# Kernel optimization log

Measured on AMD Instinct MI355X. Metric: run time of the kernel, lower is better.

The kernel has to match this reference:

```python
import jax, jax.numpy as jnp
import numpy as np

B, S, D, H, KV, HD = 2, 2048, 4096, 32, 8, 128
N_REP = H // KV


def _rope(t, fr, fi):
    # t: [b, s, h, hd]; fr/fi: [s, hd//2] broadcast as [1, s, 1, hd//2]
    t2 = t.reshape(*t.shape[:-1], -1, 2)
    tr, ti = t2[..., 0], t2[..., 1]
    fr = fr[None, :, None, :]
    fi = fi[None, :, None, :]
    orr = tr * fr - fi * ti
    oi = tr * fi + ti * fr
    return jnp.stack([orr, oi], axis=-1).reshape(t.shape)


def setup_inputs() -> dict:
    key = jax.random.key(0)
    ks = jax.random.split(key, 8)
    scale = 0.02
    x = jax.random.normal(ks[0], (B, S, D), jnp.float32)
    wq = jax.random.normal(ks[1], (H * HD, D), jnp.float32) * scale
    wk = jax.random.normal(ks[2], (KV * HD, D), jnp.float32) * scale
    wv = jax.random.normal(ks[3], (KV * HD, D), jnp.float32) * scale
    wo = jax.random.normal(ks[4], (D, H * HD), jnp.float32) * scale
    # rotary frequencies (real/imag parts of freqs_cis)
    t = jnp.arange(S, dtype=jnp.float32)
    inv = 1.0 / (10000.0 ** (jnp.arange(0, HD, 2, dtype=jnp.float32) / HD))
    ang = t[:, None] * inv[None, :]  # [S, HD//2]
    fr, fi = jnp.cos(ang), jnp.sin(ang)
    # causal mask, additive
    mask = jnp.triu(jnp.full((S, S), -1e9, jnp.float32), 1)[None, None]
    cache_k = jnp.zeros((B, S, KV, HD), jnp.float32)
    cache_v = jnp.zeros((B, S, KV, HD), jnp.float32)
    indexes = jnp.arange(S, dtype=jnp.int32)
    cache_indexes = jnp.arange(S, dtype=jnp.int32)
    return dict(x=x, wq=wq, wk=wk, wv=wv, wo=wo, fr=fr, fi=fi, mask=mask,
                cache_k=cache_k, cache_v=cache_v, indexes=indexes,
                cache_indexes=cache_indexes)


def reference(x, wq, wk, wv, wo, fr, fi, mask, cache_k, cache_v, indexes, cache_indexes):
    bsz, seqlen, _ = x.shape
    xq = jnp.einsum('bsd,ed->bse', x, wq).reshape(bsz, seqlen, H, HD)
    xk = jnp.einsum('bsd,ed->bse', x, wk).reshape(bsz, seqlen, KV, HD)
    xv = jnp.einsum('bsd,ed->bse', x, wv).reshape(bsz, seqlen, KV, HD)
    xq = _rope(xq, fr, fi)
    xk = _rope(xk, fr, fi)
    # KV-cache scatter then gather
    cache_k = cache_k.at[:, indexes].set(xk)
    cache_v = cache_v.at[:, indexes].set(xv)
    keys = cache_k[:, cache_indexes]    # [b, kv_len, KV, hd]
    values = cache_v[:, cache_indexes]
    # GQA: repeat_interleave kv heads
    keys = jnp.repeat(keys, N_REP, axis=2)      # [b, kv_len, H, hd]
    values = jnp.repeat(values, N_REP, axis=2)
    q = xq.transpose(0, 2, 1, 3)        # [b, H, s, hd]
    k = keys.transpose(0, 2, 1, 3)      # [b, H, kv, hd]
    v = values.transpose(0, 2, 1, 3)
    scores = jnp.einsum('bhqd,bhkd->bhqk', q, k) / jnp.sqrt(jnp.float32(HD))
    scores = scores + mask
    probs = jax.nn.softmax(scores.astype(jnp.float32), axis=-1).astype(q.dtype)
    out = jnp.einsum('bhqk,bhkd->bhqd', probs, v)
    out = out.transpose(0, 2, 1, 3).reshape(bsz, seqlen, H * HD)
    out = jnp.einsum('bse,de->bsd', out, wo)
    return (out, xk, xv)
```

## Files before the change

kernel.cpp:

```cpp
#include <hip/hip_runtime.h>
#include <hip/hip_bf16.h>


typedef __attribute__((ext_vector_type(8)))  short s8v;
typedef __attribute__((ext_vector_type(4)))  short s4v;
typedef __attribute__((ext_vector_type(4)))  float f4v;
typedef __attribute__((ext_vector_type(16))) float f16v;
typedef __attribute__((ext_vector_type(2)))  float f2v;
typedef __attribute__((ext_vector_type(2))) unsigned int u2v;
typedef __attribute__((ext_vector_type(4))) unsigned int u4v;

typedef __attribute__((address_space(3))) void lds_void;
typedef __attribute__((address_space(1))) void g_void;

#define GLDS16(gp, lp) __builtin_amdgcn_global_load_lds((g_void*)(gp), (lds_void*)(lp), 16, 0, 0)

__device__ __forceinline__ unsigned short f2b(float f) {
  unsigned u = __builtin_bit_cast(unsigned, f);
  u += 0x7fffu + ((u >> 16) & 1u);
  return (unsigned short)(u >> 16);
}
__device__ __forceinline__ unsigned pk2(float a, float b) {
  return (unsigned)f2b(a) | ((unsigned)f2b(b) << 16);
}
__device__ __forceinline__ float b2f(unsigned short h) {
  return __builtin_bit_cast(float, (unsigned)h << 16);
}

__device__ __forceinline__ void mfma32(f4v& d, s8v a, s8v b) {
  asm volatile("v_mfma_f32_16x16x32_bf16 %0, %1, %2, %0" : "+v"(d) : "v"(a), "v"(b));
}
__device__ __forceinline__ void mfma3216(f16v& d, s8v a, s8v b) {
  asm volatile("v_mfma_f32_32x32x16_bf16 %0, %1, %2, %0" : "+v"(d) : "v"(a), "v"(b));
}
__device__ __forceinline__ s4v tr_read(const char* p, int imm) {
  s4v r;
  asm volatile("ds_read_b64_tr_b16 %0, %1 offset:%2"
               : "=v"(r) : "v"((lds_void*)p), "n"(imm));
  return r;
}

__global__ __launch_bounds__(256) void cvt_bf16(const float* __restrict__ s,
                                                unsigned short* __restrict__ d, int n4) {
  const int i = blockIdx.x * 256 + threadIdx.x;
  if (i >= n4) return;
  f4v v = *(const f4v*)(s + (size_t)i * 4);
  u2v r;
  r.x = pk2(v[0], v[1]);
  r.y = pk2(v[2], v[3]);
  *(u2v*)(d + (size_t)i * 4) = r;
}

#define BAR      asm volatile("s_barrier" ::: "memory")
#define WLGKM    do { asm volatile("s_waitcnt lgkmcnt(0)" ::: "memory"); \
                      __builtin_amdgcn_sched_barrier(0); } while (0)
#define WVM8     do { asm volatile("s_waitcnt vmcnt(8)" ::: "memory"); \
                      __builtin_amdgcn_sched_barrier(0); } while (0)

template <int OUTB>
__global__ __launch_bounds__(512, 2) void gemm_bt8(const unsigned short* __restrict__ A,
                                                   const unsigned short* __restrict__ Bp,
                                                   void* __restrict__ Cout,
                                                   int M, int N, int Ks, int Klen,
                                                   int nTiles) {
  __shared__ __align__(16) char smem[131072];
  const int tid = threadIdx.x, lane = tid & 63, wv = tid >> 6;
  const int qi = lane & 15, g = lane >> 4;
  const int wm = wv >> 2, wn = wv & 3;

  const int nwg = gridDim.x, cpx = nwg >> 3;
  const int id = blockIdx.x;
  const int swz = (id & 7) * cpx + (id >> 3);
  const int half = swz / nTiles;
  const int tile = swz - half * nTiles;
  const int kOff = half * Klen;
  const int MT = M >> 8;
  const int m0 = (tile % MT) * 256, n0 = (tile / MT) * 256;
  const int NT = Klen >> 6;

  const int srowo = wv * 8 + (lane >> 3);
  const int scole = ((lane & 7) ^ (lane >> 3)) << 3;
  const size_t rA = (size_t)(m0 + srowo) * Ks + kOff + scole;
  const size_t rB = (size_t)(n0 + srowo) * Ks + kOff + scole;
  char* sdA = smem + wv * 1024;
  char* sdB = smem + 32768 + wv * 1024;

#define STG_A(D, H, KT) do { \
    GLDS16(A + rA + (size_t)((H)*128) * Ks + (size_t)(KT)*64,      sdA + (D)*65536 + (H)*16384); \
    GLDS16(A + rA + (size_t)((H)*128 + 64) * Ks + (size_t)(KT)*64, sdA + (D)*65536 + (H)*16384 + 8192); } while (0)
#define STG_B(D, H, KT) do { \
    GLDS16(Bp + rB + (size_t)((H)*128) * Ks + (size_t)(KT)*64,      sdB + (D)*65536 + (H)*16384); \
    GLDS16(Bp + rB + (size_t)((H)*128 + 64) * Ks + (size_t)(KT)*64, sdB + (D)*65536 + (H)*16384 + 8192); } while (0)

  const int sw = (qi & 7) << 4;
  const char* frA = smem + (wm * 128 + qi) * 128;
  const char* frB = smem + 32768 + (wn * 64 + qi) * 128;

#define RDA4(D, F0) do { _Pragma("unroll") for (int f_ = 0; f_ < 4; ++f_) \
    _Pragma("unroll") for (int k_ = 0; k_ < 2; ++k_) \
      a[(F0) + f_][k_] = *(const s8v*)(frA + (D)*65536 + ((F0) + f_) * 2048 + (((k_ << 6) + (g << 4)) ^ sw)); } while (0)
#define RDB2(D, N0) do { _Pragma("unroll") for (int n_ = 0; n_ < 2; ++n_) \
    _Pragma("unroll") for (int k_ = 0; k_ < 2; ++k_) \
      b[(N0) + n_][k_] = *(const s8v*)(frB + (D)*65536 + ((N0) + n_) * 2048 + (((k_ << 6) + (g << 4)) ^ sw)); } while (0)
#define MQUAD(F0, N0) do { __builtin_amdgcn_s_setprio(1); \
    _Pragma("unroll") for (int f_ = 0; f_ < 4; ++f_) \
    _Pragma("unroll") for (int n_ = 0; n_ < 2; ++n_) \
    _Pragma("unroll") for (int k_ = 0; k_ < 2; ++k_) \
      mfma32(acc[(F0) + f_][(N0) + n_], a[(F0) + f_][k_], b[(N0) + n_][k_]); \
    __builtin_amdgcn_s_setprio(0); } while (0)

  f4v acc[8][4];
#pragma unroll
  for (int i = 0; i < 8; ++i)
#pragma unroll
    for (int j = 0; j < 4; ++j) acc[i][j] = (f4v)0.0f;

  STG_A(0, 0, 0); STG_A(0, 1, 0); STG_B(0, 0, 0); STG_B(0, 1, 0);
  STG_A(1, 0, 1); STG_A(1, 1, 1); STG_B(1, 0, 1); STG_B(1, 1, 1);
  WVM8;
  BAR;

  s8v a[8][2], b[4][2];
#pragma unroll 1
  for (int it = 0; it < NT / 2; ++it) {
    const int t = 2 * it;
    const int k2 = (t + 2 < NT) ? t + 2 : NT - 1;
    const int k3 = (t + 3 < NT) ? t + 3 : NT - 1;
    RDA4(0, 0); RDB2(0, 0);
    WLGKM; MQUAD(0, 0); BAR;
    RDB2(0, 2);
    WLGKM; MQUAD(0, 2); BAR;
    RDA4(0, 4);
    STG_B(0, 0, k2); STG_B(0, 1, k2);
    WLGKM; MQUAD(4, 0); BAR;
    STG_A(0, 0, k2); STG_A(0, 1, k2);
    MQUAD(4, 2);
    WVM8; BAR;
    RDA4(1, 0); RDB2(1, 0);
    WLGKM; MQUAD(0, 0); BAR;
    RDB2(1, 2);
    WLGKM; MQUAD(0, 2); BAR;
    RDA4(1, 4);
    STG_B(1, 0, k3); STG_B(1, 1, k3);
    WLGKM; MQUAD(4, 0); BAR;
    STG_A(1, 0, k3); STG_A(1, 1, k3);
    MQUAD(4, 2);
    WVM8; BAR;
  }

  asm volatile("s_waitcnt vmcnt(0)" ::: "memory");
  asm volatile("s_nop 7\n\ts_nop 7" ::: "memory");
  const int r4 = g * 4;
  if (OUTB) {
    unsigned short* Cb = (unsigned short*)Cout + (size_t)half * M * N;
#pragma unroll
    for (int fm = 0; fm < 8; ++fm)
#pragma unroll
      for (int fn = 0; fn < 4; ++fn)
#pragma unroll
        for (int r = 0; r < 4; ++r)
          Cb[(size_t)(m0 + wm * 128 + fm * 16 + r4 + r) * N + (n0 + wn * 64 + fn * 16 + qi)] =
              f2b(acc[fm][fn][r]);
  } else {
    float* Cf = (float*)Cout;
#pragma unroll
    for (int fm = 0; fm < 8; ++fm)
#pragma unroll
      for (int fn = 0; fn < 4; ++fn)
#pragma unroll
        for (int r = 0; r < 4; ++r)
          Cf[(size_t)(m0 + wm * 128 + fm * 16 + r4 + r) * N + (n0 + wn * 64 + fn * 16 + qi)] =
              acc[fm][fn][r];
  }
}

__global__ __launch_bounds__(256) void rope_scatter(
    const unsigned short* __restrict__ qkvp, const float* __restrict__ fr,
    const float* __restrict__ fi,
    unsigned short* __restrict__ qb, unsigned short* __restrict__ kb,
    unsigned short* __restrict__ vbuf, float* __restrict__ xk, float* __restrict__ xv) {
  const int idx = blockIdx.x * 256 + threadIdx.x;
  const int token = idx / 3072;
  const int col2  = (idx - token * 3072) * 2;
  const int pos   = token & 2047;
  const unsigned u1 = *(const unsigned*)(qkvp + (size_t)token * 6144 + col2);
  const unsigned u2 = *(const unsigned*)(qkvp + 25165824u + (size_t)token * 6144 + col2);
  float v0 = b2f((unsigned short)u1) + b2f((unsigned short)u2);
  float v1 = b2f((unsigned short)(u1 >> 16)) + b2f((unsigned short)(u2 >> 16));
  if (col2 < 4096) {
    const int j = (col2 & 127) >> 1;
    const float cr = fr[pos * 64 + j], ci = fi[pos * 64 + j];
    const float a = v0 * cr - ci * v1;
    const float o = v0 * ci + v1 * cr;
    *(unsigned*)(qb + (size_t)token * 4096 + col2) = pk2(a, o);
  } else if (col2 < 5120) {
    const int lc = col2 - 4096;
    const int j = (lc & 127) >> 1;
    const float cr = fr[pos * 64 + j], ci = fi[pos * 64 + j];
    const float a = v0 * cr - ci * v1;
    const float o = v0 * ci + v1 * cr;
    *(unsigned*)(kb + (size_t)token * 1024 + lc) = pk2(a, o);
    f2v w; w.x = a; w.y = o;
    *(f2v*)(xk + (size_t)token * 1024 + lc) = w;
  } else {
    const int lc = col2 - 5120;
    *(unsigned*)(vbuf + (size_t)token * 1024 + lc) = pk2(v0, v1);
    f2v w; w.x = v0; w.y = v1;
    *(f2v*)(xv + (size_t)token * 1024 + lc) = w;
  }
}

#define SCL_LOG2 0.12751744f

__global__ __launch_bounds__(512, 2) void attn_fwd(
    const unsigned short* __restrict__ qb, const unsigned short* __restrict__ kb,
    const unsigned short* __restrict__ vb, unsigned short* __restrict__ ao) {
  __shared__ __align__(16) char smem[49152];
  char* const Ks = smem;
  const int tid = threadIdx.x, lane = tid & 63, wv = tid >> 6;
  const int q31 = lane & 31, hi = lane >> 5;
  const int qtb = 7 - blockIdx.x;
  const int h = blockIdx.y, b = blockIdx.z, kvh = h >> 2;
  const int q0 = qtb * 256;
  const int qrow = q0 + wv * 32 + q31;

  s8v qf[8];
  {
    const unsigned short* qp = qb + (size_t)(b * 2048 + qrow) * 4096 + h * 128 + hi * 8;
#pragma unroll
    for (int c = 0; c < 8; ++c) qf[c] = *(const s8v*)(qp + c * 16);
  }

  f16v oacc[4];
#pragma unroll
  for (int i = 0; i < 4; ++i) oacc[i] = (f16v)0.0f;
  float m_run = -3.0e38f, l_run = 0.0f;

  const unsigned short* ksrc[2]; char* kdst[2];
#pragma unroll
  for (int j = 0; j < 2; ++j) {
    const int r = wv * 8 + j * 4 + (lane >> 4);
    ksrc[j] = kb + (size_t)(b * 2048 + r) * 1024 + kvh * 128 + (((lane & 15) ^ (r & 15)) << 3);
    kdst[j] = Ks + (wv * 8 + j * 4) * 256;
  }
  const unsigned short* vsrc[2]; int vdoff[2];
#pragma unroll
  for (int j = 0; j < 2; ++j) {
    const int key = (wv * 2 + j) * 4 + ((lane & 7) >> 1);
    const int d = ((lane >> 3) & 7) * 16 + (lane & 1) * 8;
    vsrc[j] = vb + (size_t)(b * 2048 + key) * 1024 + kvh * 128 + d;
    vdoff[j] = (wv * 16 + j * 8) * 128;
  }

  const int ntiles = 4 * qtb + 4;
  const int my_qmax = q0 + wv * 32 + 31, wq_lo = q0 + wv * 32;

  GLDS16(ksrc[0], kdst[0]); GLDS16(ksrc[1], kdst[1]);
  GLDS16(vsrc[0], smem + 16384 + vdoff[0]); GLDS16(vsrc[1], smem + 16384 + vdoff[1]);
  asm volatile("s_waitcnt vmcnt(2)" ::: "memory");
  __builtin_amdgcn_sched_barrier(0);
  BAR;

  for (int t = 0; t < ntiles; ++t) {
    const int k0 = t * 64;
    const bool live = (k0 <= my_qmax);
    f16v s32a = (f16v)0.0f, s32b = (f16v)0.0f;
    if (live) {
      __builtin_amdgcn_s_setprio(1);
#pragma unroll
      for (int c = 0; c < 8; ++c) {
        const int sl = ((2 * c + hi) ^ (q31 & 15)) << 4;
        s8v kfa = *(const s8v*)(Ks + q31 * 256 + sl);
        s8v kfb = *(const s8v*)(Ks + (32 + q31) * 256 + sl);
        mfma3216(s32a, kfa, qf[c]);
        mfma3216(s32b, kfb, qf[c]);
      }
      __builtin_amdgcn_s_setprio(0);
      asm volatile("s_nop 7\n\ts_nop 7\n\ts_nop 7" : "+v"(s32a), "+v"(s32b));
    }
    BAR;
    {
      const size_t off = (size_t)((t + 1 < ntiles) ? t + 1 : t) * 65536;
      char* vbase = smem + 16384 + ((t + 1) & 1) * 16384;
      GLDS16(ksrc[0] + off, kdst[0]);
      GLDS16(ksrc[1] + off, kdst[1]);
      GLDS16(vsrc[0] + off, vbase + vdoff[0]);
      GLDS16(vsrc[1] + off, vbase + vdoff[1]);
    }
    asm volatile("s_waitcnt vmcnt(2)" ::: "memory");
    __builtin_amdgcn_sched_barrier(0);
    BAR;
    if (live) {
      const char* vbt = smem + 16384 + (t & 1) * 16384 + hi * 2048 +
                        ((lane >> 4) & 1) * 128 + ((lane & 15) << 3);
      s4v tA[8], tB[8];
#pragma unroll
      for (int u = 0; u < 8; ++u) tA[u] = tr_read(vbt, (u >> 1) * 256 + (u & 1) * 1024);

      float p[32];
#pragma unroll
      for (int r = 0; r < 16; ++r) { p[r] = s32a[r]; p[16 + r] = s32b[r]; }
      float tm = -3.0e38f;
      if (k0 + 64 <= wq_lo) {
#pragma unroll
        for (int j = 0; j < 32; ++j) { p[j] *= SCL_LOG2; tm = fmaxf(tm, p[j]); }
      } else {
#pragma unroll
        for (int j = 0; j < 32; ++j) {
          const int keyg = k0 + (j >> 4) * 32 + (j & 3) + 8 * ((j >> 2) & 3) + 4 * hi;
          p[j] = (keyg <= qrow) ? p[j] * SCL_LOG2 : -3.0e38f;
          tm = fmaxf(tm, p[j]);
        }
      }
      tm = fmaxf(tm, __shfl_xor(tm, 32));

      if (!__all(tm - m_run <= 8.0f)) {
        const float m_new = fmaxf(m_run, tm);
        const float al = exp2f(m_run - m_new);
#pragma unroll
        for (int i = 0; i < 4; ++i)
#pragma unroll
          for (int r = 0; r < 16; ++r) oacc[i][r] *= al;
        l_run *= al;
        m_run = m_new;
      }
      float ps = 0.0f;
#pragma unroll
      for (int j = 0; j < 32; ++j) { p[j] = exp2f(p[j] - m_run); ps += p[j]; }
      ps += __shfl_xor(ps, 32);
      l_run += ps;

      s8v pf[4];
#pragma unroll
      for (int ks = 0; ks < 4; ++ks) {
        unsigned c0, c1, c2, c3;
        asm("v_cvt_pk_bf16_f32 %0, %1, %2" : "=v"(c0) : "v"(p[ks*8+0]), "v"(p[ks*8+1]));
        asm("v_cvt_pk_bf16_f32 %0, %1, %2" : "=v"(c1) : "v"(p[ks*8+2]), "v"(p[ks*8+3]));
        asm("v_cvt_pk_bf16_f32 %0, %1, %2" : "=v"(c2) : "v"(p[ks*8+4]), "v"(p[ks*8+5]));
        asm("v_cvt_pk_bf16_f32 %0, %1, %2" : "=v"(c3) : "v"(p[ks*8+6]), "v"(p[ks*8+7]));
        asm volatile("v_permlane32_swap_b32 %0, %1" : "+v"(c0), "+v"(c2));
        asm volatile("v_permlane32_swap_b32 %0, %1" : "+v"(c1), "+v"(c3));
        u4v pw; pw.x = c0; pw.y = c1; pw.z = c2; pw.w = c3;
        pf[ks] = __builtin_bit_cast(s8v, pw);
      }

#define PVS(KS, CUR, NXT, LAST) do { \
        if (!(LAST)) { \
          _Pragma("unroll") for (int u = 0; u < 8; ++u) \
            NXT[u] = tr_read(vbt, ((KS)+1)*4096 + (u >> 1) * 256 + (u & 1) * 1024); \
          asm volatile("s_waitcnt lgkmcnt(8)" ::: "memory"); \
        } else { asm volatile("s_waitcnt lgkmcnt(0)" ::: "memory"); } \
        __builtin_amdgcn_sched_barrier(0); \
        __builtin_amdgcn_s_setprio(1); \
        _Pragma("unroll") for (int dt = 0; dt < 4; ++dt) { \
          s8v vf = __builtin_shufflevector(CUR[dt*2], CUR[dt*2+1], 0,1,2,3,4,5,6,7); \
          mfma3216(oacc[dt], vf, pf[KS]); } \
        __builtin_amdgcn_s_setprio(0); \
      } while (0)
      PVS(0, tA, tB, 0);
      PVS(1, tB, tA, 0);
      PVS(2, tA, tB, 0);
      PVS(3, tB, tA, 1);
#undef PVS
    }
  }

  asm volatile("s_waitcnt vmcnt(0) lgkmcnt(0)" ::: "memory");
  asm volatile("s_nop 7\n\ts_nop 7\n\ts_nop 7" ::: "memory");
  __syncthreads();
  const float inv = 1.0f / l_run;
  float* Ost = (float*)smem;
  const int er = tid >> 3, ew = (tid & 7) * 16;
#pragma unroll
  for (int pq = 0; pq < 4; ++pq) {
    if ((wv >> 1) == pq) {
      const int qip = (wv & 1) * 32 + q31;
#pragma unroll
      for (int dt = 0; dt < 4; ++dt)
#pragma unroll
        for (int r = 0; r < 16; ++r) {
          const int d = dt * 32 + (r & 3) + 8 * ((r >> 2) & 3) + 4 * hi;
          Ost[qip * 128 + (d ^ ((qip & 7) << 2))] = oacc[dt][r] * inv;
        }
    }
    __syncthreads();
    const int sw = (er & 7) << 2;
    f4v a0 = *(const f4v*)(Ost + er * 128 + ((ew + 0) ^ sw));
    f4v a1 = *(const f4v*)(Ost + er * 128 + ((ew + 4) ^ sw));
    f4v a2 = *(const f4v*)(Ost + er * 128 + ((ew + 8) ^ sw));
    f4v a3 = *(const f4v*)(Ost + er * 128 + ((ew + 12) ^ sw));
    u4v r0, r1;
    r0.x = pk2(a0[0], a0[1]); r0.y = pk2(a0[2], a0[3]);
    r0.z = pk2(a1[0], a1[1]); r0.w = pk2(a1[2], a1[3]);
    r1.x = pk2(a2[0], a2[1]); r1.y = pk2(a2[2], a2[3]);
    r1.z = pk2(a3[0], a3[1]); r1.w = pk2(a3[2], a3[3]);
    unsigned short* dst = ao + (size_t)(b * 2048 + q0 + pq * 64 + er) * 4096 + h * 128 + ew;
    *(u4v*)dst = r0;
    *(u4v*)(dst + 8) = r1;
    __syncthreads();
  }
}

extern "C" void kernel_launch(void* const* d_in, const int* in_sizes, int n_in,
                              void* d_out, int out_size, void* d_ws, size_t ws_size,
                              hipStream_t stream) {
  (void)in_sizes; (void)n_in; (void)out_size; (void)ws_size;
  const float* x  = (const float*)d_in[0];
  const float* wq = (const float*)d_in[1];
  const float* wk = (const float*)d_in[2];
  const float* wv = (const float*)d_in[3];
  const float* wo = (const float*)d_in[4];
  const float* fr = (const float*)d_in[5];
  const float* fi = (const float*)d_in[6];

  float* out = (float*)d_out;
  float* xk  = out + 16777216;
  float* xv  = xk + 4194304;

  char* ws = (char*)d_ws;
  unsigned short* xb    = (unsigned short*)(ws);
  unsigned short* wqkvb = (unsigned short*)(ws + 33554432);
  unsigned short* wob   = (unsigned short*)(ws + 83886080);
  unsigned short* qkvb  = (unsigned short*)(ws + 117440512);
  unsigned short* aob   = (unsigned short*)(ws + 117440512);
  unsigned short* qbuf  = (unsigned short*)(ws + 218103808);
  unsigned short* kbuf  = (unsigned short*)(ws + 251658240);
  unsigned short* vbuf  = (unsigned short*)(ws + 260046848);

  cvt_bf16<<<16384, 256, 0, stream>>>(x,  xb, 4194304);
  cvt_bf16<<<16384, 256, 0, stream>>>(wq, wqkvb, 4194304);
  cvt_bf16<<<4096,  256, 0, stream>>>(wk, wqkvb + 16777216, 1048576);
  cvt_bf16<<<4096,  256, 0, stream>>>(wv, wqkvb + 20971520, 1048576);
  cvt_bf16<<<16384, 256, 0, stream>>>(wo, wob, 4194304);

  gemm_bt8<1><<<768, 512, 0, stream>>>(xb, wqkvb, qkvb, 4096, 6144, 4096, 2048, 384);
  rope_scatter<<<49152, 256, 0, stream>>>(qkvb, fr, fi, qbuf, kbuf, vbuf, xk, xv);
  attn_fwd<<<dim3(8, 32, 2), 512, 0, stream>>>(qbuf, kbuf, vbuf, aob);
  gemm_bt8<0><<<256, 512, 0, stream>>>(aob, wob, out, 4096, 4096, 4096, 4096, 256);
}
```

Baseline: 610.0 us.

## Double-buffer K tiles two ahead and fold softmax scale into Q

K tiles now use two LDS buffers and are prefetched two tiles ahead, while V keeps its double buffer one tile ahead. LDS grows from 48KB to 64KB and the wait threshold is relaxed to vmcnt(4), so more load latency is hidden behind the QK and softmax work. Separately, the log2-scaled softmax factor is applied to Q in the rope kernel, which removes the per-element multiply in the attention loop. The larger LDS footprint may limit the 2-blocks-per-CU occupancy target, and scaling Q before the bf16 rounding slightly changes numerics.

After: 590.3 us. -3.2%, faster.

```diff
diff --git a/kernel.cpp b/kernel.cpp
--- a/kernel.cpp
+++ b/kernel.cpp
@@ -14,6 +14,8 @@
 typedef __attribute__((address_space(1))) void g_void;
 
 #define GLDS16(gp, lp) __builtin_amdgcn_global_load_lds((g_void*)(gp), (lds_void*)(lp), 16, 0, 0)
+
+#define SCL_LOG2 0.12751744f
 
 __device__ __forceinline__ unsigned short f2b(float f) {
   unsigned u = __builtin_bit_cast(unsigned, f);
@@ -190,8 +192,8 @@
   if (col2 < 4096) {
     const int j = (col2 & 127) >> 1;
     const float cr = fr[pos * 64 + j], ci = fi[pos * 64 + j];
-    const float a = v0 * cr - ci * v1;
-    const float o = v0 * ci + v1 * cr;
+    const float a = (v0 * cr - ci * v1) * SCL_LOG2;
+    const float o = (v0 * ci + v1 * cr) * SCL_LOG2;
     *(unsigned*)(qb + (size_t)token * 4096 + col2) = pk2(a, o);
   } else if (col2 < 5120) {
     const int lc = col2 - 4096;
@@ -210,13 +212,10 @@
   }
 }
 
-#define SCL_LOG2 0.12751744f
-
 __global__ __launch_bounds__(512, 2) void attn_fwd(
     const unsigned short* __restrict__ qb, const unsigned short* __restrict__ kb,
     const unsigned short* __restrict__ vb, unsigned short* __restrict__ ao) {
-  __shared__ __align__(16) char smem[49152];
-  char* const Ks = smem;
+  __shared__ __align__(16) char smem[65536];
   const int tid = threadIdx.x, lane = tid & 63, wv = tid >> 6;
   const int q31 = lane & 31, hi = lane >> 5;
   const int qtb = 7 - blockIdx.x;
@@ -236,42 +235,47 @@
   for (int i = 0; i < 4; ++i) oacc[i] = (f16v)0.0f;
   float m_run = -3.0e38f, l_run = 0.0f;
 
-  const unsigned short* ksrc[2]; char* kdst[2];
+  const unsigned short* ksrc[2]; int kdo[2];
 #pragma unroll
   for (int j = 0; j < 2; ++j) {
     const int r = wv * 8 + j * 4 + (lane >> 4);
     ksrc[j] = kb + (size_t)(b * 2048 + r) * 1024 + kvh * 128 + (((lane & 15) ^ (r & 15)) << 3);
-    kdst[j] = Ks + (wv * 8 + j * 4) * 256;
-  }
-  const unsigned short* vsrc[2]; int vdoff[2];
+    kdo[j] = (wv * 8 + j * 4) * 256;
+  }
+  const unsigned short* vsrc[2]; int vdo[2];
 #pragma unroll
   for (int j = 0; j < 2; ++j) {
     const int key = (wv * 2 + j) * 4 + ((lane & 7) >> 1);
     const int d = ((lane >> 3) & 7) * 16 + (lane & 1) * 8;
     vsrc[j] = vb + (size_t)(b * 2048 + key) * 1024 + kvh * 128 + d;
-    vdoff[j] = (wv * 16 + j * 8) * 128;
+    vdo[j] = (wv * 16 + j * 8) * 128;
   }
 
   const int ntiles = 4 * qtb + 4;
   const int my_qmax = q0 + wv * 32 + 31, wq_lo = q0 + wv * 32;
 
-  GLDS16(ksrc[0], kdst[0]); GLDS16(ksrc[1], kdst[1]);
-  GLDS16(vsrc[0], smem + 16384 + vdoff[0]); GLDS16(vsrc[1], smem + 16384 + vdoff[1]);
-  asm volatile("s_waitcnt vmcnt(2)" ::: "memory");
+  GLDS16(ksrc[0], smem + kdo[0]);
+  GLDS16(ksrc[1], smem + kdo[1]);
+  GLDS16(ksrc[0] + 65536, smem + 16384 + kdo[0]);
+  GLDS16(ksrc[1] + 65536, smem + 16384 + kdo[1]);
+  GLDS16(vsrc[0], smem + 32768 + vdo[0]);
+  GLDS16(vsrc[1], smem + 32768 + vdo[1]);
+  asm volatile("s_waitcnt vmcnt(4)" ::: "memory");
   __builtin_amdgcn_sched_barrier(0);
   BAR;
 
   for (int t = 0; t < ntiles; ++t) {
     const int k0 = t * 64;
     const bool live = (k0 <= my_qmax);
+    const char* Kbase = smem + (t & 1) * 16384;
     f16v s32a = (f16v)0.0f, s32b = (f16v)0.0f;
     if (live) {
       __builtin_amdgcn_s_setprio(1);
 #pragma unroll
       for (int c = 0; c < 8; ++c) {
         const int sl = ((2 * c + hi) ^ (q31 & 15)) << 4;
-        s8v kfa = *(const s8v*)(Ks + q31 * 256 + sl);
-        s8v kfb = *(const s8v*)(Ks + (32 + q31) * 256 + sl);
+        s8v kfa = *(const s8v*)(Kbase + q31 * 256 + sl);
+        s8v kfb = *(const s8v*)(Kbase + (32 + q31) * 256 + sl);
         mfma3216(s32a, kfa, qf[c]);
         mfma3216(s32b, kfb, qf[c]);
       }
@@ -280,18 +284,20 @@
     }
     BAR;
     {
-      const size_t off = (size_t)((t + 1 < ntiles) ? t + 1 : t) * 65536;
-      char* vbase = smem + 16384 + ((t + 1) & 1) * 16384;
-      GLDS16(ksrc[0] + off, kdst[0]);
-      GLDS16(ksrc[1] + off, kdst[1]);
-      GLDS16(vsrc[0] + off, vbase + vdoff[0]);
-      GLDS16(vsrc[1] + off, vbase + vdoff[1]);
+      const int kt2 = (t + 2 < ntiles) ? t + 2 : ntiles - 1;
+      const int vt1 = (t + 1 < ntiles) ? t + 1 : ntiles - 1;
+      char* kd = smem + (t & 1) * 16384;
+      char* vd = smem + 32768 + ((t + 1) & 1) * 16384;
+      GLDS16(ksrc[0] + (size_t)kt2 * 65536, kd + kdo[0]);
+      GLDS16(ksrc[1] + (size_t)kt2 * 65536, kd + kdo[1]);
+      GLDS16(vsrc[0] + (size_t)vt1 * 65536, vd + vdo[0]);
+      GLDS16(vsrc[1] + (size_t)vt1 * 65536, vd + vdo[1]);
     }
-    asm volatile("s_waitcnt vmcnt(2)" ::: "memory");
+    asm volatile("s_waitcnt vmcnt(4)" ::: "memory");
     __builtin_amdgcn_sched_barrier(0);
     BAR;
     if (live) {
-      const char* vbt = smem + 16384 + (t & 1) * 16384 + hi * 2048 +
+      const char* vbt = smem + 32768 + (t & 1) * 16384 + hi * 2048 +
                         ((lane >> 4) & 1) * 128 + ((lane & 15) << 3);
       s4v tA[8], tB[8];
 #pragma unroll
@@ -303,12 +309,12 @@
       float tm = -3.0e38f;
       if (k0 + 64 <= wq_lo) {
 #pragma unroll
-        for (int j = 0; j < 32; ++j) { p[j] *= SCL_LOG2; tm = fmaxf(tm, p[j]); }
+        for (int j = 0; j < 32; ++j) tm = fmaxf(tm, p[j]);
       } else {
 #pragma unroll
         for (int j = 0; j < 32; ++j) {
           const int keyg = k0 + (j >> 4) * 32 + (j & 3) + 8 * ((j >> 2) & 3) + 4 * hi;
-          p[j] = (keyg <= qrow) ? p[j] * SCL_LOG2 : -3.0e38f;
+          p[j] = (keyg <= qrow) ? p[j] : -3.0e38f;
           tm = fmaxf(tm, p[j]);
         }
       }
```
